# Kernel tuning notes

Hardware: AMD Instinct MI355X
Metric: run time of the kernel (lower is better)

The kernel has to match this reference:

```python
import jax, jax.numpy as jnp
import numpy as np

B, T, D, H, OUT_STEPS = 4096, 50, 64, 128, 100  # batch, warmup steps, latent dim, hidden units, rollout steps


def setup_inputs() -> dict:
    key = jax.random.key(0)
    ks = jax.random.split(key, 9)
    s = jnp.float32(0.05)  # keep gates out of saturation
    return {
        "x":   jax.random.normal(ks[0], (B, T, D), jnp.float32),
        "Wk0": jax.random.normal(ks[1], (D, 4 * H), jnp.float32) * s,
        "Wr0": jax.random.normal(ks[2], (H, 4 * H), jnp.float32) * s,
        "b0":  jax.random.normal(ks[3], (4 * H,), jnp.float32) * s,
        "Wk1": jax.random.normal(ks[4], (H, 4 * H), jnp.float32) * s,
        "Wr1": jax.random.normal(ks[5], (H, 4 * H), jnp.float32) * s,
        "b1":  jax.random.normal(ks[6], (4 * H,), jnp.float32) * s,
        "Wd":  jax.random.normal(ks[7], (H, D), jnp.float32) * s,
        "bd":  jax.random.normal(ks[8], (D,), jnp.float32) * s,
    }


def _lstm_cell(xt, h, c, Wk, Wr, b):
    # Keras LSTMCell: gates in order i, f, g(cell), o
    z = xt @ Wk + h @ Wr + b  # [B, 4H]
    i, f, g, o = jnp.split(z, 4, axis=-1)
    c_new = jax.nn.sigmoid(f) * c + jax.nn.sigmoid(i) * jnp.tanh(g)
    h_new = jax.nn.sigmoid(o) * jnp.tanh(c_new)
    return h_new, c_new


def reference(x, Wk0, Wr0, b0, Wk1, Wr1, b1, Wd, bd):
    Bn = x.shape[0]
    Hn = Wr0.shape[0]
    z = jnp.zeros((Bn, Hn), x.dtype)

    def warm_step(carry, xt):
        h0, c0, h1, c1 = carry
        h0, c0 = _lstm_cell(xt, h0, c0, Wk0, Wr0, b0)
        h1, c1 = _lstm_cell(h0, h1, c1, Wk1, Wr1, b1)
        return (h0, c0, h1, c1), None

    # warmup over the provided sequence (T >= min_warmup_steps=10)
    carry, _ = jax.lax.scan(warm_step, (z, z, z, z), jnp.swapaxes(x, 0, 1))
    pred0 = carry[2] @ Wd + bd  # Dense on last layer's hidden state

    def ar_step(carry, _):
        pred, h0, c0, h1, c1 = carry
        h0, c0 = _lstm_cell(pred, h0, c0, Wk0, Wr0, b0)
        h1, c1 = _lstm_cell(h0, h1, c1, Wk1, Wr1, b1)
        pred = h1 @ Wd + bd
        return (pred, h0, c0, h1, c1), pred

    _, preds = jax.lax.scan(ar_step, (pred0,) + carry, None, length=OUT_STEPS - 1)
    preds = jnp.concatenate([pred0[None], preds], axis=0)  # [OUT, B, D]
    return jnp.swapaxes(preds, 0, 1)  # [B, OUT, D]
```

## Files before the change

kernel.cpp:

```cpp
#include <hip/hip_runtime.h>
#include <hip/hip_bf16.h>

#define Tt   50
#define Dd   64
#define NOUT 100
#define G4   512
#define K0S  72
#define K1P  264
#define BM   16

typedef __attribute__((ext_vector_type(8))) short  short8;
typedef __attribute__((ext_vector_type(4))) float  floatx4;

#if __has_builtin(__builtin_amdgcn_exp2f)
#define EXP2(v) __builtin_amdgcn_exp2f(v)
#else
#define EXP2(v) exp2f(v)
#endif
__device__ __forceinline__ float rcp_(float v) { return __builtin_amdgcn_rcpf(v); }
__device__ __forceinline__ float fsig2(float u)  { return rcp_(1.0f + EXP2(u)); }
__device__ __forceinline__ float ftanh2(float u) { return fmaf(2.0f, rcp_(1.0f + EXP2(u)), -1.0f); }
#define KN2L2E (-2.8853900817779268f)

__device__ __forceinline__ short f2bf(float f) {
    __hip_bfloat16 h = __float2bfloat16(f);
    return *reinterpret_cast<const short*>(&h);
}

#define W1F_OFF 196608
#define WDF_OFF 458752
#define B0F_OFF 475136
#define B1F_OFF 477184
#define BDF_OFF 479232

__global__ __launch_bounds__(256) void prep_kernel(
    const float* __restrict__ Wk0, const float* __restrict__ Wr0, const float* __restrict__ b0,
    const float* __restrict__ Wk1, const float* __restrict__ Wr1, const float* __restrict__ b1,
    const float* __restrict__ Wd,  const float* __restrict__ bd,  char* __restrict__ ws)
{
    int idx = blockIdx.x * 256 + threadIdx.x;
    short* w0f = (short*)ws;
    short* w1f = (short*)(ws + W1F_OFF);
    short* wdf = (short*)(ws + WDF_OFF);
    float* b0f = (float*)(ws + B0F_OFF);
    float* b1f = (float*)(ws + B1F_OFF);
    float* bdf = (float*)(ws + BDF_OFF);
    const float NL2E = -1.4426950408889634f;
    const float N2L2E = -2.8853900817779268f;

    if (idx < 98304) {
        int f = idx >> 9, r = idx & 511;
        int lane = r >> 3, j = r & 7;
        int nt = f / 6, kt = f - nt * 6;
        int k = kt * 32 + (lane >> 4) * 8 + j;
        int col = nt * 16 + (lane & 15);
        float sc = ((col >> 7) == 2) ? N2L2E : NL2E;
        w0f[idx] = f2bf(sc * ((k < Dd) ? Wk0[k * G4 + col] : Wr0[(k - Dd) * G4 + col]));
    } else if (idx < 229376) {
        int i2 = idx - 98304;
        int f = i2 >> 9, r = i2 & 511;
        int lane = r >> 3, j = r & 7;
        int nt = f >> 3, kt = f & 7;
        int k = kt * 32 + (lane >> 4) * 8 + j;
        int col = nt * 16 + (lane & 15);
        float sc = ((col >> 7) == 2) ? N2L2E : NL2E;
        w1f[i2] = f2bf(sc * ((k < 128) ? Wk1[k * G4 + col] : Wr1[(k - 128) * G4 + col]));
    } else if (idx < 237568) {
        int i2 = idx - 229376;
        int f = i2 >> 9, r = i2 & 511;
        int lane = r >> 3, j = r & 7;
        int nt = f >> 2, kt = f & 3;
        int k = kt * 32 + (lane >> 4) * 8 + j;
        int col = nt * 16 + (lane & 15);
        wdf[i2] = f2bf(Wd[k * Dd + col]);
    } else if (idx < 237568 + 1088) {
        int i2 = idx - 237568;
        if (i2 < 512) {
            float sc = ((i2 >> 7) == 2) ? N2L2E : NL2E;
            b0f[i2] = sc * b0[i2];
        } else if (i2 < 1024) {
            int c = i2 - 512;
            float sc = ((c >> 7) == 2) ? N2L2E : NL2E;
            b1f[c] = sc * b1[c];
        } else bdf[i2 - 1024] = bd[i2 - 1024];
    }
}

#define SM_A1  4608
#define SM_W0  21504
#define SM_TOT 152576
#define A0SZ   1152
#define A1SZ   4224

__global__ __launch_bounds__(512, 2) void lstm_kernel(
    const float* __restrict__ x, const char* __restrict__ ws, float* __restrict__ out)
{
    extern __shared__ char smem[];
    short* a0b = (short*)smem;
    short* a1b = (short*)(smem + SM_A1);
    short* w0l = (short*)(smem + SM_W0);

    const short* w0f = (const short*)ws;
    const short* w1f = (const short*)(ws + W1F_OFF);
    const short* wdf = (const short*)(ws + WDF_OFF);
    const float* b0f = (const float*)(ws + B0F_OFF);
    const float* b1f = (const float*)(ws + B1F_OFF);
    const float* bdf = (const float*)(ws + BDF_OFF);

    const int tid  = threadIdx.x;
    const int w    = tid >> 6;
    const int lane = tid & 63;
    const int l15  = lane & 15;
    const int quad = lane >> 4;
    const int row0 = blockIdx.x * BM;

    for (int i = tid; i < 2 * A0SZ; i += 512) a0b[i] = 0;
    for (int i = tid; i < 2 * A1SZ; i += 512) a1b[i] = 0;
    for (int c = tid; c < 8192; c += 512) {
        int e8 = c & 63;
        int wv = (c >> 6) & 7;
        int p  = c >> 9;
        int g = p / 6, kt = p - g * 6;
        const short* src = w0f + ((((g * 8 + wv) * 6) + kt) << 9) + e8 * 8;
        *(short8*)&w0l[((p * 8 + wv) << 9) + e8 * 8] = *(const short8*)src;
    }
    {
        int colx = tid & 63, rg = tid >> 6;
        a0b[rg * K0S + colx]       = f2bf(x[(size_t)(row0 + rg) * (Tt * Dd) + colx]);
        a0b[(rg + 8) * K0S + colx] = f2bf(x[(size_t)(row0 + rg + 8) * (Tt * Dd) + colx]);
    }

    const short* w0rb = w0f + w * 3072 + lane * 8;
    const short* w1rb = w1f + w * 4096 + lane * 8;
    short8 W1R[4][8];
    #pragma unroll
    for (int g = 0; g < 4; ++g)
        #pragma unroll
        for (int kt = 0; kt < 8; ++kt)
            W1R[g][kt] = *(const short8*)(w1rb + g * 32768 + kt * 512);
    short8 W0R[8];
    #pragma unroll
    for (int p = 16; p < 24; ++p) {
        int g = p / 6, kt = p - g * 6;
        W0R[p - 16] = *(const short8*)(w0rb + g * 24576 + kt * 512);
    }
    short8 WdR[4];
    if (w < 4) {
        #pragma unroll
        for (int kt = 0; kt < 4; ++kt)
            WdR[kt] = *(const short8*)(wdf + ((w * 4 + kt) << 9) + lane * 8);
    }

    const int hu = w * 16 + l15;
    const float bi0 = b0f[hu], bff0 = b0f[128 + hu], bg0 = b0f[256 + hu], bo0 = b0f[384 + hu];
    const float bi1 = b1f[hu], bff1 = b1f[128 + hu], bg1 = b1f[256 + hu], bo1 = b1f[384 + hu];
    const float bdv = bdf[(w & 3) * 16 + l15];

    float c0s[4] = {0.f, 0.f, 0.f, 0.f};
    float c1s[4] = {0.f, 0.f, 0.f, 0.f};

    const int colx = tid & 63, rg = tid >> 6;

    __syncthreads();

    for (int step = 0; step < 149; ++step) {
        const int p = step & 1, q = p ^ 1;
        short* a0p = a0b + p * A0SZ;  short* a0q = a0b + q * A0SZ;
        short* a1p = a1b + p * A1SZ;  short* a1q = a1b + q * A1SZ;

        float xv0, xv1;
        if (step < Tt - 1) {
            xv0 = x[(size_t)(row0 + rg)     * (Tt * Dd) + (step + 1) * Dd + colx];
            xv1 = x[(size_t)(row0 + rg + 8) * (Tt * Dd) + (step + 1) * Dd + colx];
        }

        floatx4 acc[4];
        acc[0] = (floatx4){bi0,  bi0,  bi0,  bi0};
        acc[1] = (floatx4){bff0, bff0, bff0, bff0};
        acc[2] = (floatx4){bg0,  bg0,  bg0,  bg0};
        acc[3] = (floatx4){bo0,  bo0,  bo0,  bo0};

        #pragma unroll
        for (int kt = 0; kt < 6; ++kt) {
            short8 af = (kt < 2)
                ? *(const short8*)&a0p[l15 * K0S + kt * 32 + quad * 8]
                : *(const short8*)&a1q[l15 * K1P + (kt - 2) * 32 + quad * 8];
            #pragma unroll
            for (int g = 0; g < 4; ++g) {
                int pp = g * 6 + kt;
                short8 bfr = (pp < 16) ? *(const short8*)&w0l[((pp * 8 + w) << 9) + lane * 8]
                                       : W0R[pp - 16];
                acc[g] = __builtin_amdgcn_mfma_f32_16x16x32_bf16(af, bfr, acc[g], 0, 0, 0);
            }
        }

        #pragma unroll
        for (int r = 0; r < 4; ++r) {
            float si = fsig2(acc[0][r]);
            float sf = fsig2(acc[1][r]);
            float tg = ftanh2(acc[2][r]);
            float so = fsig2(acc[3][r]);
            float c  = fmaf(sf, c0s[r], si * tg);
            c0s[r] = c;
            float h  = so * ftanh2(c * KN2L2E);
            a1p[(quad * 4 + r) * K1P + hu] = f2bf(h);
        }

        if (step < Tt - 1) {
            a0q[rg * K0S + colx]       = f2bf(xv0);
            a0q[(rg + 8) * K0S + colx] = f2bf(xv1);
        }
        __syncthreads();

        acc[0] = (floatx4){bi1,  bi1,  bi1,  bi1};
        acc[1] = (floatx4){bff1, bff1, bff1, bff1};
        acc[2] = (floatx4){bg1,  bg1,  bg1,  bg1};
        acc[3] = (floatx4){bo1,  bo1,  bo1,  bo1};

        #pragma unroll
        for (int kt = 0; kt < 8; ++kt) {
            short8 af = *(const short8*)&a1p[l15 * K1P + kt * 32 + quad * 8];
            #pragma unroll
            for (int g = 0; g < 4; ++g)
                acc[g] = __builtin_amdgcn_mfma_f32_16x16x32_bf16(af, W1R[g][kt], acc[g], 0, 0, 0);
        }

        #pragma unroll
        for (int r = 0; r < 4; ++r) {
            float si = fsig2(acc[0][r]);
            float sf = fsig2(acc[1][r]);
            float tg = ftanh2(acc[2][r]);
            float so = fsig2(acc[3][r]);
            float c  = fmaf(sf, c1s[r], si * tg);
            c1s[r] = c;
            float h  = so * ftanh2(c * KN2L2E);
            a1q[(quad * 4 + r) * K1P + 128 + hu] = f2bf(h);
        }

        if (step >= Tt - 1) {
            __syncthreads();
            if (w < 4) {
                floatx4 ad = (floatx4){bdv, bdv, bdv, bdv};
                #pragma unroll
                for (int kt = 0; kt < 4; ++kt) {
                    short8 a_ = *(const short8*)&a1q[l15 * K1P + 128 + kt * 32 + quad * 8];
                    ad = __builtin_amdgcn_mfma_f32_16x16x32_bf16(a_, WdR[kt], ad, 0, 0, 0);
                }
                int s = step - (Tt - 1);
                #pragma unroll
                for (int r = 0; r < 4; ++r) {
                    float pv = ad[r];
                    int row = quad * 4 + r;
                    int col = w * 16 + l15;
                    out[(size_t)(row0 + row) * (NOUT * Dd) + s * Dd + col] = pv;
                    a0q[row * K0S + col] = f2bf(pv);
                }
            }
            __syncthreads();
        }
    }
}

extern "C" void kernel_launch(void* const* d_in, const int* in_sizes, int n_in,
                              void* d_out, int out_size, void* d_ws, size_t ws_size,
                              hipStream_t stream)
{
    (void)in_sizes; (void)n_in; (void)out_size; (void)ws_size;
    static_assert(SM_TOT <= 160 * 1024, "LDS budget");
    hipFuncSetAttribute(reinterpret_cast<const void*>(lstm_kernel),
                        hipFuncAttributeMaxDynamicSharedMemorySize, SM_TOT);
    prep_kernel<<<933, 256, 0, stream>>>(
        (const float*)d_in[1], (const float*)d_in[2], (const float*)d_in[3],
        (const float*)d_in[4], (const float*)d_in[5], (const float*)d_in[6],
        (const float*)d_in[7], (const float*)d_in[8], (char*)d_ws);
    lstm_kernel<<<256, 512, SM_TOT, stream>>>(
        (const float*)d_in[0], (const char*)d_ws, (float*)d_out);
}
```

Measured before the change: 506.0 us.

## Skew LSTM layers across steps to halve barriers during warmup

Layer 1 of step t and layer 0 of step t+1 now run in the same loop iteration, since both read the same hidden-state buffer. This lets the warmup phase use a single barrier per step instead of two and gives the scheduler more independent MFMA chains to interleave. The autoregressive phase keeps the dense-prediction dependency, so it still needs extra barriers, and separate prologue and epilogue blocks handle the skew. The cost is more register pressure from two live accumulator sets, plus more complex buffer indexing that could introduce errors.

```diff
diff --git a/kernel.cpp b/kernel.cpp
--- a/kernel.cpp
+++ b/kernel.cpp
@@ -92,6 +92,23 @@
 #define A0SZ   1152
 #define A1SZ   4224
 
+#define MFMA_B16(A, B, C) __builtin_amdgcn_mfma_f32_16x16x32_bf16((A), (B), (C), 0, 0, 0)
+
+#define W0FRAG(PP) ((PP) < 16 ? *(const short8*)&w0l[(((PP) * 8 + w) << 9) + lane * 8] \
+                              : W0R[(PP) - 16])
+
+#define GATES(ACC, CS, BASE, COLOFF)                                                     \
+    _Pragma("unroll")                                                                    \
+    for (int rr = 0; rr < 4; ++rr) {                                                     \
+        float si = fsig2(ACC[0][rr]);                                                    \
+        float sf = fsig2(ACC[1][rr]);                                                    \
+        float tg = ftanh2(ACC[2][rr]);                                                   \
+        float so = fsig2(ACC[3][rr]);                                                    \
+        float c_ = fmaf(sf, CS[rr], si * tg);                                            \
+        CS[rr] = c_;                                                                     \
+        (BASE)[(quad * 4 + rr) * K1P + (COLOFF) + hu] = f2bf(so * ftanh2(c_ * KN2L2E));  \
+    }
+
 __global__ __launch_bounds__(512, 2) void lstm_kernel(
     const float* __restrict__ x, const char* __restrict__ ws, float* __restrict__ out)
 {
@@ -124,10 +141,12 @@
         const short* src = w0f + ((((g * 8 + wv) * 6) + kt) << 9) + e8 * 8;
         *(short8*)&w0l[((p * 8 + wv) << 9) + e8 * 8] = *(const short8*)src;
     }
+    const int colx = tid & 63, rgr = tid >> 6;
     {
-        int colx = tid & 63, rg = tid >> 6;
-        a0b[rg * K0S + colx]       = f2bf(x[(size_t)(row0 + rg) * (Tt * Dd) + colx]);
-        a0b[(rg + 8) * K0S + colx] = f2bf(x[(size_t)(row0 + rg + 8) * (Tt * Dd) + colx]);
+        a0b[A0SZ + rgr * K0S + colx]       = f2bf(x[(size_t)(row0 + rgr) * (Tt * Dd) + colx]);
+        a0b[A0SZ + (rgr + 8) * K0S + colx] = f2bf(x[(size_t)(row0 + rgr + 8) * (Tt * Dd) + colx]);
+        a0b[rgr * K0S + colx]              = f2bf(x[(size_t)(row0 + rgr) * (Tt * Dd) + Dd + colx]);
+        a0b[(rgr + 8) * K0S + colx]        = f2bf(x[(size_t)(row0 + rgr + 8) * (Tt * Dd) + Dd + colx]);
     }
 
     const short* w0rb = w0f + w * 3072 + lane * 8;
@@ -159,104 +178,148 @@
     float c0s[4] = {0.f, 0.f, 0.f, 0.f};
     float c1s[4] = {0.f, 0.f, 0.f, 0.f};
 
-    const int colx = tid & 63, rg = tid >> 6;
-
     __syncthreads();
 
-    for (int step = 0; step < 149; ++step) {
-        const int p = step & 1, q = p ^ 1;
-        short* a0p = a0b + p * A0SZ;  short* a0q = a0b + q * A0SZ;
-        short* a1p = a1b + p * A1SZ;  short* a1q = a1b + q * A1SZ;
+    {
+        floatx4 acc0[4];
+        acc0[0] = (floatx4){bi0,  bi0,  bi0,  bi0};
+        acc0[1] = (floatx4){bff0, bff0, bff0, bff0};
+        acc0[2] = (floatx4){bg0,  bg0,  bg0,  bg0};
+        acc0[3] = (floatx4){bo0,  bo0,  bo0,  bo0};
+        #pragma unroll
+        for (int kt = 0; kt < 2; ++kt) {
+            short8 af = *(const short8*)&a0b[A0SZ + l15 * K0S + kt * 32 + quad * 8];
+            #pragma unroll
+            for (int g = 0; g < 4; ++g) {
+                const int pp = g * 6 + kt;
+                acc0[g] = MFMA_B16(af, W0FRAG(pp), acc0[g]);
+            }
+        }
+        GATES(acc0, c0s, a1b + A1SZ, 0);
+    }
+    __syncthreads();
+
+    for (int r = 0; r < 148; ++r) {
+        short* Rb  = a1b + (((r + 1) & 1) ? A1SZ : 0);
+        short* Wb  = a1b + ((r & 1) ? A1SZ : 0);
+        short* a0r = a0b + ((r & 1) ? A0SZ : 0);
+        short* a0w = a0b + (((r + 1) & 1) ? A0SZ : 0);
 
         float xv0, xv1;
-        if (step < Tt - 1) {
-            xv0 = x[(size_t)(row0 + rg)     * (Tt * Dd) + (step + 1) * Dd + colx];
-            xv1 = x[(size_t)(row0 + rg + 8) * (Tt * Dd) + (step + 1) * Dd + colx];
-        }
-
-        floatx4 acc[4];
-        acc[0] = (floatx4){bi0,  bi0,  bi0,  bi0};
-        acc[1] = (floatx4){bff0, bff0, bff0, bff0};
-        acc[2] = (floatx4){bg0,  bg0,  bg0,  bg0};
-        acc[3] = (floatx4){bo0,  bo0,  bo0,  bo0};
-
-        #pragma unroll
-        for (int kt = 0; kt < 6; ++kt) {
-            short8 af = (kt < 2)
-                ? *(const short8*)&a0p[l15 * K0S + kt * 32 + quad * 8]
-                : *(const short8*)&a1q[l15 * K1P + (kt - 2) * 32 + quad * 8];
+        if (r < 48) {
+            xv0 = x[(size_t)(row0 + rgr)     * (Tt * Dd) + (r + 2) * Dd + colx];
+            xv1 = x[(size_t)(row0 + rgr + 8) * (Tt * Dd) + (r + 2) * Dd + colx];
+        }
+
+        floatx4 acc1[4], acc0[4];
+        acc1[0] = (floatx4){bi1,  bi1,  bi1,  bi1};
+        acc1[1] = (floatx4){bff1, bff1, bff1, bff1};
+        acc1[2] = (floatx4){bg1,  bg1,  bg1,  bg1};
+        acc1[3] = (floatx4){bo1,  bo1,  bo1,  bo1};
+        acc0[0] = (floatx4){bi0,  bi0,  bi0,  bi0};
+        acc0[1] = (floatx4){bff0, bff0, bff0, bff0};
+        acc0[2] = (floatx4){bg0,  bg0,  bg0,  bg0};
+        acc0[3] = (floatx4){bo0,  bo0,  bo0,  bo0};
+
+        #pragma unroll
+        for (int kt = 0; kt < 8; ++kt) {
+            short8 af = *(const short8*)&Rb[l15 * K1P + kt * 32 + quad * 8];
+            #pragma unroll
+            for (int g = 0; g < 4; ++g)
+                acc1[g] = MFMA_B16(af, W1R[g][kt], acc1[g]);
+        }
+        #pragma unroll
+        for (int kt = 2; kt < 6; ++kt) {
+            short8 af = *(const short8*)&Rb[l15 * K1P + (kt - 2) * 32 + quad * 8];
             #pragma unroll
             for (int g = 0; g < 4; ++g) {
-                int pp = g * 6 + kt;
-                short8 bfr = (pp < 16) ? *(const short8*)&w0l[((pp * 8 + w) << 9) + lane * 8]
-                                       : W0R[pp - 16];
-                acc[g] = __builtin_amdgcn_mfma_f32_16x16x32_bf16(af, bfr, acc[g], 0, 0, 0);
-            }
-        }
-
-        #pragma unroll
-        for (int r = 0; r < 4; ++r) {
-            float si = fsig2(acc[0][r]);
-            float sf = fsig2(acc[1][r]);
-            float tg = ftanh2(acc[2][r]);
-            float so = fsig2(acc[3][r]);
-            float c  = fmaf(sf, c0s[r], si * tg);
-            c0s[r] = c;
-            float h  = so * ftanh2(c * KN2L2E);
-            a1p[(quad * 4 + r) * K1P + hu] = f2bf(h);
-        }
-
-        if (step < Tt - 1) {
-            a0q[rg * K0S + colx]       = f2bf(xv0);
-            a0q[(rg + 8) * K0S + colx] = f2bf(xv1);
-        }
-        __syncthreads();
-
-        acc[0] = (floatx4){bi1,  bi1,  bi1,  bi1};
-        acc[1] = (floatx4){bff1, bff1, bff1, bff1};
-        acc[2] = (floatx4){bg1,  bg1,  bg1,  bg1};
-        acc[3] = (floatx4){bo1,  bo1,  bo1,  bo1};
-
-        #pragma unroll
-        for (int kt = 0; kt < 8; ++kt) {
-            short8 af = *(const short8*)&a1p[l15 * K1P + kt * 32 + quad * 8];
-            #pragma unroll
-            for (int g = 0; g < 4; ++g)
-                acc[g] = __builtin_amdgcn_mfma_f32_16x16x32_bf16(af, W1R[g][kt], acc[g], 0, 0, 0);
-        }
-
-        #pragma unroll
-        for (int r = 0; r < 4; ++r) {
-            float si = fsig2(acc[0][r]);
-            float sf = fsig2(acc[1][r]);
-            float tg = ftanh2(acc[2][r]);
-            float so = fsig2(acc[3][r]);
-            float c  = fmaf(sf, c1s[r], si * tg);
-            c1s[r] = c;
-            float h  = so * ftanh2(c * KN2L2E);
-            a1q[(quad * 4 + r) * K1P + 128 + hu] = f2bf(h);
-        }
-
-        if (step >= Tt - 1) {
+                const int pp = g * 6 + kt;
+                acc0[g] = MFMA_B16(af, W0FRAG(pp), acc0[g]);
+            }
+        }
+
+        if (r < 49) {
+            #pragma unroll
+            for (int kt = 0; kt < 2; ++kt) {
+                short8 af = *(const short8*)&a0r[l15 * K0S + kt * 32 + quad * 8];
+                #pragma unroll
+                for (int g = 0; g < 4; ++g) {
+                    const int pp = g * 6 + kt;
+                    acc0[g] = MFMA_B16(af, W0FRAG(pp), acc0[g]);
+                }
+            }
+            GATES(acc1, c1s, Wb, 128);
+            GATES(acc0, c0s, Wb, 0);
+            if (r < 48) {
+                a0w[rgr * K0S + colx]       = f2bf(xv0);
+                a0w[(rgr + 8) * K0S + colx] = f2bf(xv1);
+            }
+            __syncthreads();
+        } else {
+            GATES(acc1, c1s, Wb, 128);
             __syncthreads();
             if (w < 4) {
                 floatx4 ad = (floatx4){bdv, bdv, bdv, bdv};
                 #pragma unroll
                 for (int kt = 0; kt < 4; ++kt) {
-                    short8 a_ = *(const short8*)&a1q[l15 * K1P + 128 + kt * 32 + quad * 8];
-                    ad = __builtin_amdgcn_mfma_f32_16x16x32_bf16(a_, WdR[kt], ad, 0, 0, 0);
+                    short8 a_ = *(const short8*)&Wb[l15 * K1P + 128 + kt * 32 + quad * 8];
+                    ad = MFMA_B16(a_, WdR[kt], ad);
                 }
-                int s = step - (Tt - 1);
+                const int s = r - 49;
                 #pragma unroll
-                for (int r = 0; r < 4; ++r) {
-                    float pv = ad[r];
-                    int row = quad * 4 + r;
+                for (int rr = 0; rr < 4; ++rr) {
+                    float pv = ad[rr];
+                    int row = quad * 4 + rr;
                     int col = w * 16 + l15;
                     out[(size_t)(row0 + row) * (NOUT * Dd) + s * Dd + col] = pv;
-                    a0q[row * K0S + col] = f2bf(pv);
+                    a0b[row * K0S + col] = f2bf(pv);
                 }
             }
             __syncthreads();
+            #pragma unroll
+            for (int kt = 0; kt < 2; ++kt) {
+                short8 af = *(const short8*)&a0b[l15 * K0S + kt * 32 + quad * 8];
+                #pragma unroll
+                for (int g = 0; g < 4; ++g) {
+                    const int pp = g * 6 + kt;
+                    acc0[g] = MFMA_B16(af, W0FRAG(pp), acc0[g]);
+                }
+            }
+            GATES(acc0, c0s, Wb, 0);
+            __syncthreads();
+        }
+    }
+
+    {
+        short* Rb = a1b + A1SZ;
+        short* Wb = a1b;
+        floatx4 acc1[4];
+        acc1[0] = (floatx4){bi1,  bi1,  bi1,  bi1};
+        acc1[1] = (floatx4){bff1, bff1, bff1, bff1};
+        acc1[2] = (floatx4){bg1,  bg1,  bg1,  bg1};
+        acc1[3] = (floatx4){bo1,  bo1,  bo1,  bo1};
+        #pragma unroll
+        for (int kt = 0; kt < 8; ++kt) {
+            short8 af = *(const short8*)&Rb[l15 * K1P + kt * 32 + quad * 8];
+            #pragma unroll
+            for (int g = 0; g < 4; ++g)
+                acc1[g] = MFMA_B16(af, W1R[g][kt], acc1[g]);
+        }
+        GATES(acc1, c1s, Wb, 128);
+        __syncthreads();
+        if (w < 4) {
+            floatx4 ad = (floatx4){bdv, bdv, bdv, bdv};
+            #pragma unroll
+            for (int kt = 0; kt < 4; ++kt) {
+                short8 a_ = *(const short8*)&Wb[l15 * K1P + 128 + kt * 32 + quad * 8];
+                ad = MFMA_B16(a_, WdR[kt], ad);
+            }
+            #pragma unroll
+            for (int rr = 0; rr < 4; ++rr) {
+                int row = quad * 4 + rr;
+                int col = w * 16 + l15;
+                out[(size_t)(row0 + row) * (NOUT * Dd) + 99 * Dd + col] = ad[rr];
+            }
         }
     }
 }
```

Result: slower. 672.8 us (+33.0%).
